# Kernel tuning notes

Measured on AMD Instinct MI355X. Metric: run time of the kernel, lower is better.

## Reference

```python
import jax, jax.numpy as jnp
import numpy as np

SEQ_LS = [512, 512, 512, 512]
HEADS = 8
DIM_HEAD = 64
DIM = 512
INNER = HEADS * DIM_HEAD  # 512
N = sum(SEQ_LS)           # 2048
B = 4
EPS = 1e-5

# static modality id per token position: [N]
MOD_IDS = jnp.asarray(np.repeat(np.arange(len(SEQ_LS)), SEQ_LS))


def setup_inputs() -> dict:
    key = jax.random.key(0)
    ks = jax.random.split(key, 6)
    x = jax.random.normal(ks[0], (B, N, DIM), dtype=jnp.float32)
    m_labels = jnp.ones((B, len(SEQ_LS)), dtype=jnp.int64 if jax.config.jax_enable_x64 else jnp.int32)
    gamma = jnp.ones((DIM,), dtype=jnp.float32)
    beta = jnp.zeros((DIM,), dtype=jnp.float32)
    w_qkv = jax.random.normal(ks[1], (DIM, 3 * INNER), dtype=jnp.float32) * (DIM ** -0.5)
    w_out = jax.random.normal(ks[2], (INNER, DIM), dtype=jnp.float32) * (INNER ** -0.5)
    b_out = jnp.zeros((DIM,), dtype=jnp.float32)
    return {"x": x, "m_labels": m_labels, "gamma": gamma, "beta": beta,
            "w_qkv": w_qkv, "w_out": w_out, "b_out": b_out}


def _additive_mask(m_labels):
    # present[b, n] = modality of token n is present in sample b
    present = (m_labels[:, MOD_IDS] != 0)                       # [B, N] bool
    pair_ok = present[:, :, None] & present[:, None, :]         # [B, N, N]
    neg_inf = jnp.float32(-jnp.inf)
    return jnp.where(pair_ok, jnp.float32(0.0), neg_inf)        # [B, N, N]


def reference(x, m_labels, gamma, beta, w_qkv, w_out, b_out):
    # LayerNorm(dim)
    mu = jnp.mean(x, axis=-1, keepdims=True)
    var = jnp.mean(jnp.square(x - mu), axis=-1, keepdims=True)
    xn = (x - mu) * jax.lax.rsqrt(var + EPS) * gamma + beta

    # QKV projection (no bias), split heads
    qkv = jnp.einsum('bnd,de->bne', xn, w_qkv)                  # [B, N, 3*INNER]
    q, k, v = jnp.split(qkv, 3, axis=-1)
    def heads(t):
        return t.reshape(B, N, HEADS, DIM_HEAD).transpose(0, 2, 1, 3)  # [B, H, N, Dh]
    q, k, v = heads(q), heads(k), heads(v)

    scale = DIM_HEAD ** -0.5
    dots = jnp.einsum('bhnd,bhmd->bhnm', q, k) * scale          # [B, H, N, N]
    dots = dots + _additive_mask(m_labels)[:, None, :, :]
    attn = jax.nn.softmax(dots, axis=-1)
    out = jnp.einsum('bhnm,bhmd->bhnd', attn, v)                # [B, H, N, Dh]
    out = out.transpose(0, 2, 1, 3).reshape(B, N, INNER)        # [B, N, INNER]
    return jnp.einsum('bni,io->bno', out, w_out) + b_out        # [B, N, DIM]
```

## Files before the change

kernel.cpp:

```cpp
#include <hip/hip_runtime.h>

#define DIMD 512
#define NTOK 2048
#define HEADS 8
#define DH 64

typedef __attribute__((ext_vector_type(4))) float f32x4;
typedef __attribute__((ext_vector_type(8))) __bf16 bf16x8;
typedef __attribute__((ext_vector_type(4))) short s16x4;

#define MFMA16(a, b, c) __builtin_amdgcn_mfma_f32_16x16x32_bf16((a), (b), (c), 0, 0, 0)
#define MFMAK16(a, b, c) __builtin_amdgcn_mfma_f32_16x16x16bf16_1k((a), (b), (c), 0, 0, 0)

__device__ __forceinline__ unsigned short f2bf(float f) {
  unsigned int u = __float_as_uint(f);
  u += 0x7fffu + ((u >> 16) & 1u);
  return (unsigned short)(u >> 16);
}

__device__ __forceinline__ unsigned packhi(float b, float a) {
  return (__float_as_uint(b) >> 16) | (__float_as_uint(a) & 0xffff0000u);
}

__device__ __forceinline__ void gl2lds16(const void* g, void* l) {
  auto gp = reinterpret_cast<__attribute__((address_space(1))) unsigned int*>(
      reinterpret_cast<unsigned long long>(g));
  auto lp = reinterpret_cast<__attribute__((address_space(3))) unsigned int*>(
      reinterpret_cast<unsigned long long>(l));
  __builtin_amdgcn_global_load_lds(gp, lp, 16, 0, 0);
}

__global__ __launch_bounds__(256) void ln_kernel(const float* __restrict__ x,
                                                 const float* __restrict__ gamma,
                                                 const float* __restrict__ beta,
                                                 unsigned short* __restrict__ xn) {
  const int row = blockIdx.x * 4 + (threadIdx.x >> 6);
  const int lane = threadIdx.x & 63;
  const float4* xr = (const float4*)(x + (size_t)row * DIMD);
  float4 a = xr[lane];
  float4 b = xr[lane + 64];
  float s = a.x + a.y + a.z + a.w + b.x + b.y + b.z + b.w;
  for (int off = 1; off < 64; off <<= 1) s += __shfl_xor(s, off, 64);
  float mu = s * (1.0f / DIMD);
  float d0 = a.x - mu, d1 = a.y - mu, d2 = a.z - mu, d3 = a.w - mu;
  float e0 = b.x - mu, e1 = b.y - mu, e2 = b.z - mu, e3 = b.w - mu;
  float v = d0 * d0 + d1 * d1 + d2 * d2 + d3 * d3 + e0 * e0 + e1 * e1 + e2 * e2 + e3 * e3;
  for (int off = 1; off < 64; off <<= 1) v += __shfl_xor(v, off, 64);
  float rs = rsqrtf(v * (1.0f / DIMD) + 1e-5f);
  const float4* g4 = (const float4*)gamma;
  const float4* be4 = (const float4*)beta;
  float4 ga = g4[lane], gb = g4[lane + 64];
  float4 ba = be4[lane], bb = be4[lane + 64];
  unsigned int p0 = (unsigned)f2bf(d0 * rs * ga.x + ba.x) | ((unsigned)f2bf(d1 * rs * ga.y + ba.y) << 16);
  unsigned int p1 = (unsigned)f2bf(d2 * rs * ga.z + ba.z) | ((unsigned)f2bf(d3 * rs * ga.w + ba.w) << 16);
  unsigned int p2 = (unsigned)f2bf(e0 * rs * gb.x + bb.x) | ((unsigned)f2bf(e1 * rs * gb.y + bb.y) << 16);
  unsigned int p3 = (unsigned)f2bf(e2 * rs * gb.z + bb.z) | ((unsigned)f2bf(e3 * rs * gb.w + bb.w) << 16);
  uint2 w0; w0.x = p0; w0.y = p1;
  uint2 w1; w1.x = p2; w1.y = p3;
  *(uint2*)&xn[(size_t)row * DIMD + lane * 4] = w0;
  *(uint2*)&xn[(size_t)row * DIMD + 256 + lane * 4] = w1;
}

__global__ __launch_bounds__(256) void wt_kernel(const float* __restrict__ w,
                                                 unsigned short* __restrict__ wt,
                                                 int R, int C) {
  __shared__ float t[32][33];
  int tx = threadIdx.x & 31, ty = threadIdx.x >> 5;
  int c0 = blockIdx.x * 32, r0 = blockIdx.y * 32;
  for (int i = 0; i < 4; i++)
    t[ty + 8 * i][tx] = w[(size_t)(r0 + ty + 8 * i) * C + c0 + tx];
  __syncthreads();
  for (int i = 0; i < 4; i++)
    wt[(size_t)(c0 + ty + 8 * i) * R + r0 + tx] = f2bf(t[tx][ty + 8 * i]);
}

__global__ __launch_bounds__(256, 2) void qkv_gemm(const unsigned short* __restrict__ A,
                                                   const unsigned short* __restrict__ Bt,
                                                   unsigned short* __restrict__ qb,
                                                   unsigned short* __restrict__ kb,
                                                   unsigned short* __restrict__ vtb) {
  __shared__ unsigned short As[2][128 * 64];
  __shared__ unsigned short Bs[2][128 * 64];
  const int tid = threadIdx.x;
  const int wave = tid >> 6, lane = tid & 63;
  const int row16 = lane & 15, quad = lane >> 4;
  const int rho = row16 & 7;
  const int m0 = blockIdx.x * 128;
  const int n0 = blockIdx.y * 128;
  const int rw = (wave & 1) * 64, cw = (wave >> 1) * 64;

  const char* Ab = (const char*)A;
  const char* Bb = (const char*)Bt;
#pragma unroll
  for (int i = 0; i < 4; i++) {
    int idx = i * 256 + tid;
    int r = idx >> 3;
    int c = (idx & 7) ^ (r & 7);
    gl2lds16(Ab + ((size_t)(m0 + r) * DIMD) * 2 + c * 16, (char*)As[0] + idx * 16);
    gl2lds16(Bb + ((size_t)(n0 + r) * DIMD) * 2 + c * 16, (char*)Bs[0] + idx * 16);
  }
  __syncthreads();

  f32x4 acc[4][4] = {};
  for (int kt = 0; kt < 8; kt++) {
    const int buf = kt & 1;
    if (kt < 7) {
      const int k0 = (kt + 1) * 64;
#pragma unroll
      for (int i = 0; i < 4; i++) {
        int idx = i * 256 + tid;
        int r = idx >> 3;
        int c = (idx & 7) ^ (r & 7);
        gl2lds16(Ab + ((size_t)(m0 + r) * DIMD + k0) * 2 + c * 16, (char*)As[buf ^ 1] + idx * 16);
        gl2lds16(Bb + ((size_t)(n0 + r) * DIMD + k0) * 2 + c * 16, (char*)Bs[buf ^ 1] + idx * 16);
      }
    }
#pragma unroll
    for (int ks = 0; ks < 2; ks++) {
      bf16x8 av[4], bv[4];
#pragma unroll
      for (int i = 0; i < 4; i++) {
        int Ra = rw + i * 16 + row16;
        int Rb = cw + i * 16 + row16;
        av[i] = *(const bf16x8*)&As[buf][Ra * 64 + (((ks * 4 + quad) ^ rho) * 8)];
        bv[i] = *(const bf16x8*)&Bs[buf][Rb * 64 + (((ks * 4 + quad) ^ rho) * 8)];
      }
#pragma unroll
      for (int i = 0; i < 4; i++)
#pragma unroll
        for (int j = 0; j < 4; j++) acc[i][j] = MFMA16(av[i], bv[j], acc[i][j]);
    }
    __syncthreads();
  }

  unsigned short* Ct = (unsigned short*)As;
#pragma unroll
  for (int i = 0; i < 4; i++)
#pragma unroll
    for (int j = 0; j < 4; j++)
#pragma unroll
      for (int r = 0; r < 4; r++)
        Ct[(rw + i * 16 + quad * 4 + r) * 136 + cw + j * 16 + row16] = f2bf(acc[i][j][r]);
  __syncthreads();

  const int sect = n0 >> 9;
  const int h0 = (n0 & 511) >> 6;
  const int b = m0 >> 11;
  const int nbase = m0 & 2047;
  if (sect < 2) {
    unsigned short* dst = (sect == 0) ? qb : kb;
#pragma unroll
    for (int i = 0; i < 8; i++) {
      int cid = i * 256 + tid;
      int row = cid >> 4, col0 = (cid & 15) * 8;
      int h = h0 + (col0 >> 6), d0 = col0 & 63;
      uint4 val = *(const uint4*)&Ct[row * 136 + col0];
      *(uint4*)&dst[(((size_t)(b * HEADS + h) * NTOK) + nbase + row) * DH + d0] = val;
    }
  } else {
#pragma unroll
    for (int u = 0; u < 4; u++) {
      int uid = u * 256 + tid;
      int col = uid >> 3, rc = (uid & 7) * 16;
      int h = h0 + (col >> 6), d = col & 63;
      unsigned short tmp[16];
#pragma unroll
      for (int j = 0; j < 16; j++) tmp[j] = Ct[(rc + j) * 136 + col];
      size_t base = ((size_t)(b * HEADS + h) * DH + d) * NTOK + nbase + rc;
      *(uint4*)&vtb[base] = *(uint4*)&tmp[0];
      *(uint4*)&vtb[base + 8] = *(uint4*)&tmp[8];
    }
  }
}

__global__ __launch_bounds__(256, 2) void attn_kernel(const unsigned short* __restrict__ qb,
                                                      const unsigned short* __restrict__ kb,
                                                      const unsigned short* __restrict__ vtb,
                                                      const int* __restrict__ mlab,
                                                      unsigned short* __restrict__ ao) {
  __shared__ unsigned short Qs[128 * 64];
  __shared__ unsigned short Ks[2][64 * 64];
  __shared__ unsigned short Vs[2][64 * 64];
  const int tid = threadIdx.x;
  const int wave = tid >> 6, lane = tid & 63;
  const int row16 = lane & 15, quad = lane >> 4;
  const int rho = row16 & 7;
  const int bh = blockIdx.y;
  const int b = bh >> 3, h = bh & 7;
  const int q0 = blockIdx.x * 128;

  const char* qg = (const char*)(qb + ((size_t)bh * NTOK + q0) * DH);
  const char* kgb = (const char*)(kb + (size_t)bh * NTOK * DH);
  const char* vgb = (const char*)(vtb + (size_t)bh * DH * NTOK);
  const int sr = tid >> 3;
  const int sc = (tid & 7) ^ (sr & 7);

#pragma unroll
  for (int i = 0; i < 4; i++)
    gl2lds16(qg + (sr + 32 * i) * 128 + sc * 16, (char*)Qs + tid * 16 + i * 4096);
  gl2lds16(kgb + sr * 128 + sc * 16, (char*)Ks[0] + tid * 16);
  gl2lds16(kgb + (sr + 32) * 128 + sc * 16, (char*)Ks[0] + tid * 16 + 4096);
  gl2lds16(vgb + (size_t)sr * 4096 + sc * 16, (char*)Vs[0] + tid * 16);
  gl2lds16(vgb + (size_t)(sr + 32) * 4096 + sc * 16, (char*)Vs[0] + tid * 16 + 4096);
  __syncthreads();

  bf16x8 aq[2][2];
#pragma unroll
  for (int qs = 0; qs < 2; qs++) {
    const int qrow = wave * 32 + qs * 16 + row16;
#pragma unroll
    for (int ki = 0; ki < 2; ki++)
      aq[qs][ki] = *(const bf16x8*)&Qs[qrow * 64 + (((ki * 4 + quad) ^ rho) * 8)];
  }

  f32x4 accT[4][2] = {};
  float lsum[2] = {0.f, 0.f};
  const float cs = 0.125f * 1.44269504088896f;
  const float c0 = mlab[b * 4 + 0] ? -16.f : -100000.f;
  const float c1 = mlab[b * 4 + 1] ? -16.f : -100000.f;
  const float c2 = mlab[b * 4 + 2] ? -16.f : -100000.f;
  const float c3 = mlab[b * 4 + 3] ? -16.f : -100000.f;

  for (int t = 0; t < 32; t++) {
    const int buf = t & 1;
    if (t < 31) {
      const char* kg = kgb + (size_t)(t + 1) * 8192;
      char* lk = (char*)Ks[buf ^ 1];
      gl2lds16(kg + sr * 128 + sc * 16, lk + tid * 16);
      gl2lds16(kg + (sr + 32) * 128 + sc * 16, lk + tid * 16 + 4096);
      const char* vg = vgb + (size_t)(t + 1) * 128;
      char* lv = (char*)Vs[buf ^ 1];
      gl2lds16(vg + (size_t)sr * 4096 + sc * 16, lv + tid * 16);
      gl2lds16(vg + (size_t)(sr + 32) * 4096 + sc * 16, lv + tid * 16 + 4096);
    }
    f32x4 S[2][4];
#pragma unroll
    for (int f = 0; f < 4; f++) {
      const unsigned short* Kr = &Ks[buf][(f * 16 + row16) * 64];
      bf16x8 ak0 = *(const bf16x8*)&Kr[(quad ^ rho) * 8];
      bf16x8 ak1 = *(const bf16x8*)&Kr[((quad + 4) ^ rho) * 8];
#pragma unroll
      for (int qs = 0; qs < 2; qs++) {
        f32x4 z = {};
        z = MFMA16(ak0, aq[qs][0], z);
        z = MFMA16(ak1, aq[qs][1], z);
        S[qs][f] = z;
      }
    }
    const int mi = t >> 3;
    const float c = (mi == 0) ? c0 : (mi == 1) ? c1 : (mi == 2) ? c2 : c3;
    s16x4 pf[2][4];
#pragma unroll
    for (int qs = 0; qs < 2; qs++)
#pragma unroll
      for (int f = 0; f < 4; f++) {
        float p0 = exp2f(fmaf(S[qs][f][0], cs, c));
        float p1 = exp2f(fmaf(S[qs][f][1], cs, c));
        float p2 = exp2f(fmaf(S[qs][f][2], cs, c));
        float p3 = exp2f(fmaf(S[qs][f][3], cs, c));
        lsum[qs] += (p0 + p1) + (p2 + p3);
        uint2 pk;
        pk.x = packhi(p0, p1);
        pk.y = packhi(p2, p3);
        pf[qs][f] = *(s16x4*)&pk;
      }
#pragma unroll
    for (int g = 0; g < 4; g++) {
      const unsigned short* Vr = &Vs[buf][(g * 16 + row16) * 64];
#pragma unroll
      for (int u = 0; u < 4; u++) {
        s16x4 va = *(const s16x4*)&Vr[(((2 * u + (quad >> 1)) ^ rho) * 8) + (quad & 1) * 4];
#pragma unroll
        for (int qs = 0; qs < 2; qs++) accT[g][qs] = MFMAK16(va, pf[qs][u], accT[g][qs]);
      }
    }
    __syncthreads();
  }

#pragma unroll
  for (int qs = 0; qs < 2; qs++) {
    float s = lsum[qs];
    s += __shfl_xor(s, 16, 64);
    s += __shfl_xor(s, 32, 64);
    lsum[qs] = 1.0f / s;
  }
#pragma unroll
  for (int qs = 0; qs < 2; qs++) {
    const int q = q0 + wave * 32 + qs * 16 + row16;
    unsigned short* aor = ao + ((size_t)b * NTOK + q) * DIMD + h * DH;
#pragma unroll
    for (int g = 0; g < 4; g++)
#pragma unroll
      for (int r = 0; r < 4; r++)
        aor[g * 16 + quad * 4 + r] = f2bf(accT[g][qs][r] * lsum[qs]);
  }
}

__global__ __launch_bounds__(256, 2) void out_gemm(const unsigned short* __restrict__ A,
                                                   const unsigned short* __restrict__ Bt,
                                                   const float* __restrict__ bias,
                                                   float* __restrict__ out) {
  __shared__ unsigned short As[2][128 * 64];
  __shared__ unsigned short Bs[2][128 * 64];
  const int tid = threadIdx.x;
  const int wave = tid >> 6, lane = tid & 63;
  const int row16 = lane & 15, quad = lane >> 4;
  const int rho = row16 & 7;
  const int m0 = blockIdx.x * 128;
  const int n0 = blockIdx.y * 128;
  const int rw = (wave & 1) * 64, cw = (wave >> 1) * 64;

  const char* Ab = (const char*)A;
  const char* Bb = (const char*)Bt;
#pragma unroll
  for (int i = 0; i < 4; i++) {
    int idx = i * 256 + tid;
    int r = idx >> 3;
    int c = (idx & 7) ^ (r & 7);
    gl2lds16(Ab + ((size_t)(m0 + r) * DIMD) * 2 + c * 16, (char*)As[0] + idx * 16);
    gl2lds16(Bb + ((size_t)(n0 + r) * DIMD) * 2 + c * 16, (char*)Bs[0] + idx * 16);
  }
  __syncthreads();

  f32x4 acc[4][4] = {};
  for (int kt = 0; kt < 8; kt++) {
    const int buf = kt & 1;
    if (kt < 7) {
      const int k0 = (kt + 1) * 64;
#pragma unroll
      for (int i = 0; i < 4; i++) {
        int idx = i * 256 + tid;
        int r = idx >> 3;
        int c = (idx & 7) ^ (r & 7);
        gl2lds16(Ab + ((size_t)(m0 + r) * DIMD + k0) * 2 + c * 16, (char*)As[buf ^ 1] + idx * 16);
        gl2lds16(Bb + ((size_t)(n0 + r) * DIMD + k0) * 2 + c * 16, (char*)Bs[buf ^ 1] + idx * 16);
      }
    }
#pragma unroll
    for (int ks = 0; ks < 2; ks++) {
      bf16x8 av[4], bv[4];
#pragma unroll
      for (int i = 0; i < 4; i++) {
        int Ra = rw + i * 16 + row16;
        int Rb = cw + i * 16 + row16;
        av[i] = *(const bf16x8*)&As[buf][Ra * 64 + (((ks * 4 + quad) ^ rho) * 8)];
        bv[i] = *(const bf16x8*)&Bs[buf][Rb * 64 + (((ks * 4 + quad) ^ rho) * 8)];
      }
#pragma unroll
      for (int i = 0; i < 4; i++)
#pragma unroll
        for (int j = 0; j < 4; j++) acc[i][j] = MFMA16(av[i], bv[j], acc[i][j]);
    }
    __syncthreads();
  }

#pragma unroll
  for (int j = 0; j < 4; j++) {
    const int col = n0 + cw + j * 16 + row16;
    const float bv = bias[col];
#pragma unroll
    for (int i = 0; i < 4; i++)
#pragma unroll
      for (int r = 0; r < 4; r++) {
        const int row = m0 + rw + i * 16 + quad * 4 + r;
        out[(size_t)row * DIMD + col] = acc[i][j][r] + bv;
      }
  }
}

extern "C" void kernel_launch(void* const* d_in, const int* in_sizes, int n_in,
                              void* d_out, int out_size, void* d_ws, size_t ws_size,
                              hipStream_t stream) {
  const float* x = (const float*)d_in[0];
  const int* mlab = (const int*)d_in[1];
  const float* gamma = (const float*)d_in[2];
  const float* beta = (const float*)d_in[3];
  const float* w_qkv = (const float*)d_in[4];
  const float* w_out = (const float*)d_in[5];
  const float* b_out = (const float*)d_in[6];
  float* out = (float*)d_out;

  char* ws = (char*)d_ws;
  unsigned short* xn = (unsigned short*)(ws);
  unsigned short* wqkvT = (unsigned short*)(ws + 8388608);
  unsigned short* woutT = (unsigned short*)(ws + 9961472);
  unsigned short* qbuf = (unsigned short*)(ws + 10485760);
  unsigned short* kbuf = (unsigned short*)(ws + 18874368);
  unsigned short* vtbuf = (unsigned short*)(ws + 27262976);
  unsigned short* aobuf = (unsigned short*)(ws + 35651584);

  ln_kernel<<<2048, 256, 0, stream>>>(x, gamma, beta, xn);
  wt_kernel<<<dim3(48, 16), 256, 0, stream>>>(w_qkv, wqkvT, 512, 1536);
  wt_kernel<<<dim3(16, 16), 256, 0, stream>>>(w_out, woutT, 512, 512);
  qkv_gemm<<<dim3(64, 12), 256, 0, stream>>>(xn, wqkvT, qbuf, kbuf, vtbuf);
  attn_kernel<<<dim3(16, 32), 256, 0, stream>>>(qbuf, kbuf, vtbuf, mlab, aobuf);
  out_gemm<<<dim3(64, 4), 256, 0, stream>>>(aobuf, woutT, b_out, out);
}
```

Before: 178.4 us.

## Split attention over key halves, merge prep kernels, and shrink out-GEMM tiles

Three launches (layernorm and two weight transposes) are merged into one prep kernel. Attention is split into two halves along the key axis, which doubles the grid and relies on the fixed -16 softmax offset so no max rescale is needed. The Q staging buffer is dropped so more blocks fit per CU, and a new combine kernel sums the partials and normalises. The output GEMM uses 128x64 tiles to launch more blocks. This costs an extra kernel, extra partial-output traffic, and truncating bf16 rounding of the unnormalised partials.

New measurement: 173.0 us. 1.03x faster.

```diff
diff --git a/kernel.cpp b/kernel.cpp
--- a/kernel.cpp
+++ b/kernel.cpp
@@ -21,6 +21,8 @@
 __device__ __forceinline__ unsigned packhi(float b, float a) {
   return (__float_as_uint(b) >> 16) | (__float_as_uint(a) & 0xffff0000u);
 }
+__device__ __forceinline__ float lo16(unsigned u) { return __uint_as_float(u << 16); }
+__device__ __forceinline__ float hi16(unsigned u) { return __uint_as_float(u & 0xffff0000u); }
 
 __device__ __forceinline__ void gl2lds16(const void* g, void* l) {
   auto gp = reinterpret_cast<__attribute__((address_space(1))) unsigned int*>(
@@ -30,48 +32,57 @@
   __builtin_amdgcn_global_load_lds(gp, lp, 16, 0, 0);
 }
 
-__global__ __launch_bounds__(256) void ln_kernel(const float* __restrict__ x,
-                                                 const float* __restrict__ gamma,
-                                                 const float* __restrict__ beta,
-                                                 unsigned short* __restrict__ xn) {
-  const int row = blockIdx.x * 4 + (threadIdx.x >> 6);
-  const int lane = threadIdx.x & 63;
-  const float4* xr = (const float4*)(x + (size_t)row * DIMD);
-  float4 a = xr[lane];
-  float4 b = xr[lane + 64];
-  float s = a.x + a.y + a.z + a.w + b.x + b.y + b.z + b.w;
-  for (int off = 1; off < 64; off <<= 1) s += __shfl_xor(s, off, 64);
-  float mu = s * (1.0f / DIMD);
-  float d0 = a.x - mu, d1 = a.y - mu, d2 = a.z - mu, d3 = a.w - mu;
-  float e0 = b.x - mu, e1 = b.y - mu, e2 = b.z - mu, e3 = b.w - mu;
-  float v = d0 * d0 + d1 * d1 + d2 * d2 + d3 * d3 + e0 * e0 + e1 * e1 + e2 * e2 + e3 * e3;
-  for (int off = 1; off < 64; off <<= 1) v += __shfl_xor(v, off, 64);
-  float rs = rsqrtf(v * (1.0f / DIMD) + 1e-5f);
-  const float4* g4 = (const float4*)gamma;
-  const float4* be4 = (const float4*)beta;
-  float4 ga = g4[lane], gb = g4[lane + 64];
-  float4 ba = be4[lane], bb = be4[lane + 64];
-  unsigned int p0 = (unsigned)f2bf(d0 * rs * ga.x + ba.x) | ((unsigned)f2bf(d1 * rs * ga.y + ba.y) << 16);
-  unsigned int p1 = (unsigned)f2bf(d2 * rs * ga.z + ba.z) | ((unsigned)f2bf(d3 * rs * ga.w + ba.w) << 16);
-  unsigned int p2 = (unsigned)f2bf(e0 * rs * gb.x + bb.x) | ((unsigned)f2bf(e1 * rs * gb.y + bb.y) << 16);
-  unsigned int p3 = (unsigned)f2bf(e2 * rs * gb.z + bb.z) | ((unsigned)f2bf(e3 * rs * gb.w + bb.w) << 16);
-  uint2 w0; w0.x = p0; w0.y = p1;
-  uint2 w1; w1.x = p2; w1.y = p3;
-  *(uint2*)&xn[(size_t)row * DIMD + lane * 4] = w0;
-  *(uint2*)&xn[(size_t)row * DIMD + 256 + lane * 4] = w1;
-}
-
-__global__ __launch_bounds__(256) void wt_kernel(const float* __restrict__ w,
-                                                 unsigned short* __restrict__ wt,
-                                                 int R, int C) {
+__global__ __launch_bounds__(256) void prep_kernel(const float* __restrict__ x,
+                                                   const float* __restrict__ gamma,
+                                                   const float* __restrict__ beta,
+                                                   const float* __restrict__ w_qkv,
+                                                   const float* __restrict__ w_out,
+                                                   unsigned short* __restrict__ xn,
+                                                   unsigned short* __restrict__ wqkvT,
+                                                   unsigned short* __restrict__ woutT) {
   __shared__ float t[32][33];
-  int tx = threadIdx.x & 31, ty = threadIdx.x >> 5;
-  int c0 = blockIdx.x * 32, r0 = blockIdx.y * 32;
-  for (int i = 0; i < 4; i++)
-    t[ty + 8 * i][tx] = w[(size_t)(r0 + ty + 8 * i) * C + c0 + tx];
-  __syncthreads();
-  for (int i = 0; i < 4; i++)
-    wt[(size_t)(c0 + ty + 8 * i) * R + r0 + tx] = f2bf(t[tx][ty + 8 * i]);
+  const int bid = blockIdx.x;
+  if (bid < 2048) {
+    const int row = bid * 4 + (threadIdx.x >> 6);
+    const int lane = threadIdx.x & 63;
+    const float4* xr = (const float4*)(x + (size_t)row * DIMD);
+    float4 a = xr[lane];
+    float4 b = xr[lane + 64];
+    float s = a.x + a.y + a.z + a.w + b.x + b.y + b.z + b.w;
+    for (int off = 1; off < 64; off <<= 1) s += __shfl_xor(s, off, 64);
+    float mu = s * (1.0f / DIMD);
+    float d0 = a.x - mu, d1 = a.y - mu, d2 = a.z - mu, d3 = a.w - mu;
+    float e0 = b.x - mu, e1 = b.y - mu, e2 = b.z - mu, e3 = b.w - mu;
+    float v = d0 * d0 + d1 * d1 + d2 * d2 + d3 * d3 + e0 * e0 + e1 * e1 + e2 * e2 + e3 * e3;
+    for (int off = 1; off < 64; off <<= 1) v += __shfl_xor(v, off, 64);
+    float rs = rsqrtf(v * (1.0f / DIMD) + 1e-5f);
+    const float4* g4 = (const float4*)gamma;
+    const float4* be4 = (const float4*)beta;
+    float4 ga = g4[lane], gb = g4[lane + 64];
+    float4 ba = be4[lane], bb = be4[lane + 64];
+    unsigned p0 = (unsigned)f2bf(d0 * rs * ga.x + ba.x) | ((unsigned)f2bf(d1 * rs * ga.y + ba.y) << 16);
+    unsigned p1 = (unsigned)f2bf(d2 * rs * ga.z + ba.z) | ((unsigned)f2bf(d3 * rs * ga.w + ba.w) << 16);
+    unsigned p2 = (unsigned)f2bf(e0 * rs * gb.x + bb.x) | ((unsigned)f2bf(e1 * rs * gb.y + bb.y) << 16);
+    unsigned p3 = (unsigned)f2bf(e2 * rs * gb.z + bb.z) | ((unsigned)f2bf(e3 * rs * gb.w + bb.w) << 16);
+    uint2 w0; w0.x = p0; w0.y = p1;
+    uint2 w1; w1.x = p2; w1.y = p3;
+    *(uint2*)&xn[(size_t)row * DIMD + lane * 4] = w0;
+    *(uint2*)&xn[(size_t)row * DIMD + 256 + lane * 4] = w1;
+  } else {
+    const float* w;
+    unsigned short* wt;
+    int C, bx, by;
+    if (bid < 2816) { w = w_qkv; wt = wqkvT; C = 1536; bx = (bid - 2048) % 48; by = (bid - 2048) / 48; }
+    else            { w = w_out; wt = woutT; C = 512;  bx = (bid - 2816) % 16; by = (bid - 2816) / 16; }
+    const int R = 512;
+    int tx = threadIdx.x & 31, ty = threadIdx.x >> 5;
+    int c0 = bx * 32, r0 = by * 32;
+    for (int i = 0; i < 4; i++)
+      t[ty + 8 * i][tx] = w[(size_t)(r0 + ty + 8 * i) * C + c0 + tx];
+    __syncthreads();
+    for (int i = 0; i < 4; i++)
+      wt[(size_t)(c0 + ty + 8 * i) * R + r0 + tx] = f2bf(t[tx][ty + 8 * i]);
+  }
 }
 
 __global__ __launch_bounds__(256, 2) void qkv_gemm(const unsigned short* __restrict__ A,
@@ -173,12 +184,13 @@
   }
 }
 
-__global__ __launch_bounds__(256, 2) void attn_kernel(const unsigned short* __restrict__ qb,
+__global__ __launch_bounds__(256, 4) void attn_kernel(const unsigned short* __restrict__ qb,
                                                       const unsigned short* __restrict__ kb,
                                                       const unsigned short* __restrict__ vtb,
                                                       const int* __restrict__ mlab,
-                                                      unsigned short* __restrict__ ao) {
-  __shared__ unsigned short Qs[128 * 64];
+                                                      unsigned short* __restrict__ aoP0,
+                                                      unsigned short* __restrict__ aoP1,
+                                                      float* __restrict__ lsumP) {
   __shared__ unsigned short Ks[2][64 * 64];
   __shared__ unsigned short Vs[2][64 * 64];
   const int tid = threadIdx.x;
@@ -186,44 +198,46 @@
   const int row16 = lane & 15, quad = lane >> 4;
   const int rho = row16 & 7;
   const int bh = blockIdx.y;
-  const int b = bh >> 3, h = bh & 7;
+  const int b = bh >> 3;
   const int q0 = blockIdx.x * 128;
+  const int kh = blockIdx.z;
 
   const char* qg = (const char*)(qb + ((size_t)bh * NTOK + q0) * DH);
-  const char* kgb = (const char*)(kb + (size_t)bh * NTOK * DH);
-  const char* vgb = (const char*)(vtb + (size_t)bh * DH * NTOK);
+  const char* kgb = (const char*)(kb + ((size_t)bh * NTOK + kh * 1024) * DH);
+  const char* vgb = (const char*)(vtb + (size_t)bh * DH * NTOK + kh * 1024);
   const int sr = tid >> 3;
   const int sc = (tid & 7) ^ (sr & 7);
 
-#pragma unroll
-  for (int i = 0; i < 4; i++)
-    gl2lds16(qg + (sr + 32 * i) * 128 + sc * 16, (char*)Qs + tid * 16 + i * 4096);
+  gl2lds16(qg + sr * 128 + sc * 16, (char*)Ks[1] + tid * 16);
+  gl2lds16(qg + (sr + 32) * 128 + sc * 16, (char*)Ks[1] + tid * 16 + 4096);
+  gl2lds16(qg + (sr + 64) * 128 + sc * 16, (char*)Vs[1] + tid * 16);
+  gl2lds16(qg + (sr + 96) * 128 + sc * 16, (char*)Vs[1] + tid * 16 + 4096);
   gl2lds16(kgb + sr * 128 + sc * 16, (char*)Ks[0] + tid * 16);
   gl2lds16(kgb + (sr + 32) * 128 + sc * 16, (char*)Ks[0] + tid * 16 + 4096);
   gl2lds16(vgb + (size_t)sr * 4096 + sc * 16, (char*)Vs[0] + tid * 16);
   gl2lds16(vgb + (size_t)(sr + 32) * 4096 + sc * 16, (char*)Vs[0] + tid * 16 + 4096);
   __syncthreads();
 
+  const unsigned short* Qbase = (wave < 2) ? Ks[1] : Vs[1];
   bf16x8 aq[2][2];
 #pragma unroll
   for (int qs = 0; qs < 2; qs++) {
-    const int qrow = wave * 32 + qs * 16 + row16;
+    const int rowb = (wave & 1) * 32 + qs * 16 + row16;
 #pragma unroll
     for (int ki = 0; ki < 2; ki++)
-      aq[qs][ki] = *(const bf16x8*)&Qs[qrow * 64 + (((ki * 4 + quad) ^ rho) * 8)];
-  }
+      aq[qs][ki] = *(const bf16x8*)&Qbase[rowb * 64 + (((ki * 4 + quad) ^ rho) * 8)];
+  }
+  __syncthreads();
 
   f32x4 accT[4][2] = {};
   float lsum[2] = {0.f, 0.f};
   const float cs = 0.125f * 1.44269504088896f;
-  const float c0 = mlab[b * 4 + 0] ? -16.f : -100000.f;
-  const float c1 = mlab[b * 4 + 1] ? -16.f : -100000.f;
-  const float c2 = mlab[b * 4 + 2] ? -16.f : -100000.f;
-  const float c3 = mlab[b * 4 + 3] ? -16.f : -100000.f;
-
-  for (int t = 0; t < 32; t++) {
+  const float cA = mlab[b * 4 + kh * 2] ? -16.f : -100000.f;
+  const float cB = mlab[b * 4 + kh * 2 + 1] ? -16.f : -100000.f;
+
+  for (int t = 0; t < 16; t++) {
     const int buf = t & 1;
-    if (t < 31) {
+    if (t < 15) {
       const char* kg = kgb + (size_t)(t + 1) * 8192;
       char* lk = (char*)Ks[buf ^ 1];
       gl2lds16(kg + sr * 128 + sc * 16, lk + tid * 16);
@@ -247,8 +261,7 @@
         S[qs][f] = z;
       }
     }
-    const int mi = t >> 3;
-    const float c = (mi == 0) ? c0 : (mi == 1) ? c1 : (mi == 2) ? c2 : c3;
+    const float c = (t < 8) ? cA : cB;
     s16x4 pf[2][4];
 #pragma unroll
     for (int qs = 0; qs < 2; qs++)
@@ -282,18 +295,49 @@
     float s = lsum[qs];
     s += __shfl_xor(s, 16, 64);
     s += __shfl_xor(s, 32, 64);
-    lsum[qs] = 1.0f / s;
-  }
+    lsum[qs] = s;
+  }
+  float* lsP = lsumP + (size_t)kh * 65536 + (size_t)bh * 2048 + q0;
+  if (quad == 0) {
+    lsP[wave * 32 + row16] = lsum[0];
+    lsP[wave * 32 + 16 + row16] = lsum[1];
+  }
+  unsigned short* aoPk = (kh == 0) ? aoP0 : aoP1;
 #pragma unroll
   for (int qs = 0; qs < 2; qs++) {
-    const int q = q0 + wave * 32 + qs * 16 + row16;
-    unsigned short* aor = ao + ((size_t)b * NTOK + q) * DIMD + h * DH;
-#pragma unroll
-    for (int g = 0; g < 4; g++)
-#pragma unroll
-      for (int r = 0; r < 4; r++)
-        aor[g * 16 + quad * 4 + r] = f2bf(accT[g][qs][r] * lsum[qs]);
-  }
+    const int q = wave * 32 + qs * 16 + row16;
+    unsigned short* dst = aoPk + ((size_t)bh * NTOK + q0 + q) * DH;
+#pragma unroll
+    for (int g = 0; g < 4; g++) {
+      *(unsigned*)&dst[g * 16 + quad * 4] = packhi(accT[g][qs][0], accT[g][qs][1]);
+      *(unsigned*)&dst[g * 16 + quad * 4 + 2] = packhi(accT[g][qs][2], accT[g][qs][3]);
+    }
+  }
+}
+
+__global__ __launch_bounds__(256) void combine_kernel(const unsigned short* __restrict__ aoP0,
+                                                      const unsigned short* __restrict__ aoP1,
+                                                      const float* __restrict__ lsumP,
+                                                      unsigned short* __restrict__ ao) {
+  const int idx = blockIdx.x * 256 + threadIdx.x;
+  const int d0 = (idx & 7) * 8;
+  const int h = (idx >> 3) & 7;
+  const int n = (idx >> 6) & 2047;
+  const int b = idx >> 17;
+  const size_t bhn = ((size_t)(b * 8 + h)) * 2048 + n;
+  const uint4 u1 = *(const uint4*)&aoP0[bhn * 64 + d0];
+  const uint4 u2 = *(const uint4*)&aoP1[bhn * 64 + d0];
+  const float inv = 1.0f / (lsumP[bhn] + lsumP[65536 + bhn]);
+  const unsigned* a1 = (const unsigned*)&u1;
+  const unsigned* a2 = (const unsigned*)&u2;
+  unsigned o[4];
+#pragma unroll
+  for (int k = 0; k < 4; k++) {
+    float e0 = (lo16(a1[k]) + lo16(a2[k])) * inv;
+    float e1 = (hi16(a1[k]) + hi16(a2[k])) * inv;
+    o[k] = (unsigned)f2bf(e0) | ((unsigned)f2bf(e1) << 16);
+  }
+  *(uint4*)&ao[(((size_t)b * 2048 + n) * 512) + h * 64 + d0] = *(uint4*)o;
 }
 
 __global__ __launch_bounds__(256, 2) void out_gemm(const unsigned short* __restrict__ A,
@@ -301,14 +345,14 @@
                                                    const float* __restrict__ bias,
                                                    float* __restrict__ out) {
   __shared__ unsigned short As[2][128 * 64];
-  __shared__ unsigned short Bs[2][128 * 64];
+  __shared__ unsigned short Bs[2][64 * 64];
   const int tid = threadIdx.x;
   const int wave = tid >> 6, lane = tid & 63;
   const int row16 = lane & 15, quad = lane >> 4;
   const int rho = row16 & 7;
   const int m0 = blockIdx.x * 128;
-  const int n0 = blockIdx.y * 128;
-  const int rw = (wave & 1) * 64, cw = (wave >> 1) * 64;
+  const int n0 = blockIdx.y * 64;
+  const int rw = (wave & 1) * 64, cw = (wave >> 1) * 32;
 
   const char* Ab = (const char*)A;
   const char* Bb = (const char*)Bt;
@@ -318,11 +362,17 @@
     int r = idx >> 3;
     int c = (idx & 7) ^ (r & 7);
     gl2lds16(Ab + ((size_t)(m0 + r) * DIMD) * 2 + c * 16, (char*)As[0] + idx * 16);
+  }
+#pragma unroll
+  for (int i = 0; i < 2; i++) {
+    int idx = i * 256 + tid;
+    int r = idx >> 3;
+    int c = (idx & 7) ^ (r & 7);
     gl2lds16(Bb + ((size_t)(n0 + r) * DIMD) * 2 + c * 16, (char*)Bs[0] + idx * 16);
   }
   __syncthreads();
 
-  f32x4 acc[4][4] = {};
+  f32x4 acc[4][2] = {};
   for (int kt = 0; kt < 8; kt++) {
     const int buf = kt & 1;
     if (kt < 7) {
@@ -333,29 +383,34 @@
         int r = idx >> 3;
         int c = (idx & 7) ^ (r & 7);
         gl2lds16(Ab + ((size_t)(m0 + r) * DIMD + k0) * 2 + c * 16, (char*)As[buf ^ 1] + idx * 16);
+      }
+#pragma unroll
+      for (int i = 0; i < 2; i++) {
+        int idx = i * 256 + tid;
+        int r = idx >> 3;
+        int c = (idx & 7) ^ (r & 7);
         gl2lds16(Bb + ((size_t)(n0 + r) * DIMD + k0) * 2 + c * 16, (char*)Bs[buf ^ 1] + idx * 16);
       }
     }
 #pragma unroll
     for (int ks = 0; ks < 2; ks++) {
-      bf16x8 av[4], bv[4];
-#pragma unroll
-      for (int i = 0; i < 4; i++) {
-        int Ra = rw + i * 16 + row16;
-        int Rb = cw + i * 16 + row16;
-        av[i] = *(const bf16x8*)&As[buf][Ra * 64 + (((ks * 4 + quad) ^ rho) * 8)];
-        bv[i] = *(const bf16x8*)&Bs[buf][Rb * 64 + (((ks * 4 + quad) ^ rho) * 8)];
-      }
+      bf16x8 av[4], bv[2];
 #pragma unroll
       for (int i = 0; i < 4; i++)
-#pragma unroll
-        for (int j = 0; j < 4; j++) acc[i][j] = MFMA16(av[i], bv[j], acc[i][j]);
+        av[i] = *(const bf16x8*)&As[buf][(rw + i * 16 + row16) * 64 + (((ks * 4 + quad) ^ rho) * 8)];
+#pragma unroll
+      for (int j = 0; j < 2; j++)
+        bv[j] = *(const bf16x8*)&Bs[buf][(cw + j * 16 + row16) * 64 + (((ks * 4 + quad) ^ rho) * 8)];
+#pragma unroll
+      for (int i = 0; i < 4; i++)
+#pragma unroll
+        for (int j = 0; j < 2; j++) acc[i][j] = MFMA16(av[i], bv[j], acc[i][j]);
     }
     __syncthreads();
   }
 
 #pragma unroll
-  for (int j = 0; j < 4; j++) {
+  for (int j = 0; j < 2; j++) {
     const int col = n0 + cw + j * 16 + row16;
     const float bv = bias[col];
 #pragma unroll
@@ -387,12 +442,14 @@
   unsigned short* qbuf = (unsigned short*)(ws + 10485760);
   unsigned short* kbuf = (unsigned short*)(ws + 18874368);
   unsigned short* vtbuf = (unsigned short*)(ws + 27262976);
-  unsigned short* aobuf = (unsigned short*)(ws + 35651584);
-
-  ln_kernel<<<2048, 256, 0, stream>>>(x, gamma, beta, xn);
-  wt_kernel<<<dim3(48, 16), 256, 0, stream>>>(w_qkv, wqkvT, 512, 1536);
-  wt_kernel<<<dim3(16, 16), 256, 0, stream>>>(w_out, woutT, 512, 512);
+  unsigned short* aoP1 = (unsigned short*)(ws + 35651584);
+  unsigned short* aoP0 = xn;
+  float* lsumP = (float*)wqkvT;
+  unsigned short* ao8 = qbuf;
+
+  prep_kernel<<<3072, 256, 0, stream>>>(x, gamma, beta, w_qkv, w_out, xn, wqkvT, woutT);
   qkv_gemm<<<dim3(64, 12), 256, 0, stream>>>(xn, wqkvT, qbuf, kbuf, vtbuf);
-  attn_kernel<<<dim3(16, 32), 256, 0, stream>>>(qbuf, kbuf, vtbuf, mlab, aobuf);
-  out_gemm<<<dim3(64, 4), 256, 0, stream>>>(aobuf, woutT, b_out, out);
-}
+  attn_kernel<<<dim3(16, 32, 2), 256, 0, stream>>>(qbuf, kbuf, vtbuf, mlab, aoP0, aoP1, lsumP);
+  combine_kernel<<<2048, 256, 0, stream>>>(aoP0, aoP1, lsumP, ao8);
+  out_gemm<<<dim3(64, 8), 256, 0, stream>>>(ao8, woutT, b_out, out);
+}
```

## Fuse prep kernels, compute softmax row sums via MFMA, shrink out_gemm tile

Applied to the files above, without the earlier changes.

Merges the LayerNorm and the two weight-transpose kernels into one launch, which removes two launch gaps. In attention, the per-lane exp sum and its cross-lane shuffles are replaced by an MFMA against a vector of ones, and the bf16 output stores become packed 32-bit writes that use perm-based truncation. out_gemm uses 128x64 tiles so it launches 512 blocks instead of 256, giving better CU occupancy. The trade-offs are extra MFMA work per tile, and the attention output now truncates to bf16 instead of rounding.

After: 170.2 us. 1.05x faster.

```diff
diff --git a/kernel.cpp b/kernel.cpp
--- a/kernel.cpp
+++ b/kernel.cpp
@@ -19,7 +19,11 @@
 }
 
 __device__ __forceinline__ unsigned packhi(float b, float a) {
+#if __has_builtin(__builtin_amdgcn_perm)
+  return __builtin_amdgcn_perm(__float_as_uint(a), __float_as_uint(b), 0x07060302u);
+#else
   return (__float_as_uint(b) >> 16) | (__float_as_uint(a) & 0xffff0000u);
+#endif
 }
 
 __device__ __forceinline__ void gl2lds16(const void* g, void* l) {
@@ -30,48 +34,57 @@
   __builtin_amdgcn_global_load_lds(gp, lp, 16, 0, 0);
 }
 
-__global__ __launch_bounds__(256) void ln_kernel(const float* __restrict__ x,
-                                                 const float* __restrict__ gamma,
-                                                 const float* __restrict__ beta,
-                                                 unsigned short* __restrict__ xn) {
-  const int row = blockIdx.x * 4 + (threadIdx.x >> 6);
-  const int lane = threadIdx.x & 63;
-  const float4* xr = (const float4*)(x + (size_t)row * DIMD);
-  float4 a = xr[lane];
-  float4 b = xr[lane + 64];
-  float s = a.x + a.y + a.z + a.w + b.x + b.y + b.z + b.w;
-  for (int off = 1; off < 64; off <<= 1) s += __shfl_xor(s, off, 64);
-  float mu = s * (1.0f / DIMD);
-  float d0 = a.x - mu, d1 = a.y - mu, d2 = a.z - mu, d3 = a.w - mu;
-  float e0 = b.x - mu, e1 = b.y - mu, e2 = b.z - mu, e3 = b.w - mu;
-  float v = d0 * d0 + d1 * d1 + d2 * d2 + d3 * d3 + e0 * e0 + e1 * e1 + e2 * e2 + e3 * e3;
-  for (int off = 1; off < 64; off <<= 1) v += __shfl_xor(v, off, 64);
-  float rs = rsqrtf(v * (1.0f / DIMD) + 1e-5f);
-  const float4* g4 = (const float4*)gamma;
-  const float4* be4 = (const float4*)beta;
-  float4 ga = g4[lane], gb = g4[lane + 64];
-  float4 ba = be4[lane], bb = be4[lane + 64];
-  unsigned int p0 = (unsigned)f2bf(d0 * rs * ga.x + ba.x) | ((unsigned)f2bf(d1 * rs * ga.y + ba.y) << 16);
-  unsigned int p1 = (unsigned)f2bf(d2 * rs * ga.z + ba.z) | ((unsigned)f2bf(d3 * rs * ga.w + ba.w) << 16);
-  unsigned int p2 = (unsigned)f2bf(e0 * rs * gb.x + bb.x) | ((unsigned)f2bf(e1 * rs * gb.y + bb.y) << 16);
-  unsigned int p3 = (unsigned)f2bf(e2 * rs * gb.z + bb.z) | ((unsigned)f2bf(e3 * rs * gb.w + bb.w) << 16);
-  uint2 w0; w0.x = p0; w0.y = p1;
-  uint2 w1; w1.x = p2; w1.y = p3;
-  *(uint2*)&xn[(size_t)row * DIMD + lane * 4] = w0;
-  *(uint2*)&xn[(size_t)row * DIMD + 256 + lane * 4] = w1;
-}
-
-__global__ __launch_bounds__(256) void wt_kernel(const float* __restrict__ w,
-                                                 unsigned short* __restrict__ wt,
-                                                 int R, int C) {
+__global__ __launch_bounds__(256) void prep_kernel(const float* __restrict__ x,
+                                                   const float* __restrict__ gamma,
+                                                   const float* __restrict__ beta,
+                                                   const float* __restrict__ w_qkv,
+                                                   const float* __restrict__ w_out,
+                                                   unsigned short* __restrict__ xn,
+                                                   unsigned short* __restrict__ wqkvT,
+                                                   unsigned short* __restrict__ woutT) {
   __shared__ float t[32][33];
-  int tx = threadIdx.x & 31, ty = threadIdx.x >> 5;
-  int c0 = blockIdx.x * 32, r0 = blockIdx.y * 32;
-  for (int i = 0; i < 4; i++)
-    t[ty + 8 * i][tx] = w[(size_t)(r0 + ty + 8 * i) * C + c0 + tx];
-  __syncthreads();
-  for (int i = 0; i < 4; i++)
-    wt[(size_t)(c0 + ty + 8 * i) * R + r0 + tx] = f2bf(t[tx][ty + 8 * i]);
+  const int bid = blockIdx.x;
+  if (bid < 2048) {
+    const int row = bid * 4 + (threadIdx.x >> 6);
+    const int lane = threadIdx.x & 63;
+    const float4* xr = (const float4*)(x + (size_t)row * DIMD);
+    float4 a = xr[lane];
+    float4 b = xr[lane + 64];
+    float s = a.x + a.y + a.z + a.w + b.x + b.y + b.z + b.w;
+    for (int off = 1; off < 64; off <<= 1) s += __shfl_xor(s, off, 64);
+    float mu = s * (1.0f / DIMD);
+    float d0 = a.x - mu, d1 = a.y - mu, d2 = a.z - mu, d3 = a.w - mu;
+    float e0 = b.x - mu, e1 = b.y - mu, e2 = b.z - mu, e3 = b.w - mu;
+    float v = d0 * d0 + d1 * d1 + d2 * d2 + d3 * d3 + e0 * e0 + e1 * e1 + e2 * e2 + e3 * e3;
+    for (int off = 1; off < 64; off <<= 1) v += __shfl_xor(v, off, 64);
+    float rs = rsqrtf(v * (1.0f / DIMD) + 1e-5f);
+    const float4* g4 = (const float4*)gamma;
+    const float4* be4 = (const float4*)beta;
+    float4 ga = g4[lane], gb = g4[lane + 64];
+    float4 ba = be4[lane], bb = be4[lane + 64];
+    unsigned p0 = (unsigned)f2bf(d0 * rs * ga.x + ba.x) | ((unsigned)f2bf(d1 * rs * ga.y + ba.y) << 16);
+    unsigned p1 = (unsigned)f2bf(d2 * rs * ga.z + ba.z) | ((unsigned)f2bf(d3 * rs * ga.w + ba.w) << 16);
+    unsigned p2 = (unsigned)f2bf(e0 * rs * gb.x + bb.x) | ((unsigned)f2bf(e1 * rs * gb.y + bb.y) << 16);
+    unsigned p3 = (unsigned)f2bf(e2 * rs * gb.z + bb.z) | ((unsigned)f2bf(e3 * rs * gb.w + bb.w) << 16);
+    uint2 w0; w0.x = p0; w0.y = p1;
+    uint2 w1; w1.x = p2; w1.y = p3;
+    *(uint2*)&xn[(size_t)row * DIMD + lane * 4] = w0;
+    *(uint2*)&xn[(size_t)row * DIMD + 256 + lane * 4] = w1;
+  } else {
+    const float* w;
+    unsigned short* wt;
+    int C, bx, by;
+    if (bid < 2816) { w = w_qkv; wt = wqkvT; C = 1536; bx = (bid - 2048) % 48; by = (bid - 2048) / 48; }
+    else            { w = w_out; wt = woutT; C = 512;  bx = (bid - 2816) % 16; by = (bid - 2816) / 16; }
+    const int R = 512;
+    int tx = threadIdx.x & 31, ty = threadIdx.x >> 5;
+    int c0 = bx * 32, r0 = by * 32;
+    for (int i = 0; i < 4; i++)
+      t[ty + 8 * i][tx] = w[(size_t)(r0 + ty + 8 * i) * C + c0 + tx];
+    __syncthreads();
+    for (int i = 0; i < 4; i++)
+      wt[(size_t)(c0 + ty + 8 * i) * R + r0 + tx] = f2bf(t[tx][ty + 8 * i]);
+  }
 }
 
 __global__ __launch_bounds__(256, 2) void qkv_gemm(const unsigned short* __restrict__ A,
@@ -213,8 +226,11 @@
       aq[qs][ki] = *(const bf16x8*)&Qs[qrow * 64 + (((ki * 4 + quad) ^ rho) * 8)];
   }
 
+  s16x4 onesf;
+  onesf[0] = onesf[1] = onesf[2] = onesf[3] = (short)0x3F80;
+
   f32x4 accT[4][2] = {};
-  float lsum[2] = {0.f, 0.f};
+  f32x4 accL[2] = {};
   const float cs = 0.125f * 1.44269504088896f;
   const float c0 = mlab[b * 4 + 0] ? -16.f : -100000.f;
   const float c1 = mlab[b * 4 + 1] ? -16.f : -100000.f;
@@ -258,7 +274,6 @@
         float p1 = exp2f(fmaf(S[qs][f][1], cs, c));
         float p2 = exp2f(fmaf(S[qs][f][2], cs, c));
         float p3 = exp2f(fmaf(S[qs][f][3], cs, c));
-        lsum[qs] += (p0 + p1) + (p2 + p3);
         uint2 pk;
         pk.x = packhi(p0, p1);
         pk.y = packhi(p2, p3);
@@ -274,25 +289,25 @@
         for (int qs = 0; qs < 2; qs++) accT[g][qs] = MFMAK16(va, pf[qs][u], accT[g][qs]);
       }
     }
+#pragma unroll
+    for (int u = 0; u < 4; u++)
+#pragma unroll
+      for (int qs = 0; qs < 2; qs++) accL[qs] = MFMAK16(onesf, pf[qs][u], accL[qs]);
     __syncthreads();
   }
 
-#pragma unroll
-  for (int qs = 0; qs < 2; qs++) {
-    float s = lsum[qs];
-    s += __shfl_xor(s, 16, 64);
-    s += __shfl_xor(s, 32, 64);
-    lsum[qs] = 1.0f / s;
-  }
+  float inv[2];
+  inv[0] = 1.0f / accL[0][0];
+  inv[1] = 1.0f / accL[1][0];
 #pragma unroll
   for (int qs = 0; qs < 2; qs++) {
     const int q = q0 + wave * 32 + qs * 16 + row16;
     unsigned short* aor = ao + ((size_t)b * NTOK + q) * DIMD + h * DH;
 #pragma unroll
-    for (int g = 0; g < 4; g++)
-#pragma unroll
-      for (int r = 0; r < 4; r++)
-        aor[g * 16 + quad * 4 + r] = f2bf(accT[g][qs][r] * lsum[qs]);
+    for (int g = 0; g < 4; g++) {
+      *(unsigned*)&aor[g * 16 + quad * 4] = packhi(accT[g][qs][0] * inv[qs], accT[g][qs][1] * inv[qs]);
+      *(unsigned*)&aor[g * 16 + quad * 4 + 2] = packhi(accT[g][qs][2] * inv[qs], accT[g][qs][3] * inv[qs]);
+    }
   }
 }
 
@@ -301,14 +316,14 @@
                                                    const float* __restrict__ bias,
                                                    float* __restrict__ out) {
   __shared__ unsigned short As[2][128 * 64];
-  __shared__ unsigned short Bs[2][128 * 64];
+  __shared__ unsigned short Bs[2][64 * 64];
   const int tid = threadIdx.x;
   const int wave = tid >> 6, lane = tid & 63;
   const int row16 = lane & 15, quad = lane >> 4;
   const int rho = row16 & 7;
   const int m0 = blockIdx.x * 128;
-  const int n0 = blockIdx.y * 128;
-  const int rw = (wave & 1) * 64, cw = (wave >> 1) * 64;
+  const int n0 = blockIdx.y * 64;
+  const int rw = (wave & 1) * 64, cw = (wave >> 1) * 32;
 
   const char* Ab = (const char*)A;
   const char* Bb = (const char*)Bt;
@@ -318,11 +333,17 @@
     int r = idx >> 3;
     int c = (idx & 7) ^ (r & 7);
     gl2lds16(Ab + ((size_t)(m0 + r) * DIMD) * 2 + c * 16, (char*)As[0] + idx * 16);
+  }
+#pragma unroll
+  for (int i = 0; i < 2; i++) {
+    int idx = i * 256 + tid;
+    int r = idx >> 3;
+    int c = (idx & 7) ^ (r & 7);
     gl2lds16(Bb + ((size_t)(n0 + r) * DIMD) * 2 + c * 16, (char*)Bs[0] + idx * 16);
   }
   __syncthreads();
 
-  f32x4 acc[4][4] = {};
+  f32x4 acc[4][2] = {};
   for (int kt = 0; kt < 8; kt++) {
     const int buf = kt & 1;
     if (kt < 7) {
@@ -333,29 +354,34 @@
         int r = idx >> 3;
         int c = (idx & 7) ^ (r & 7);
         gl2lds16(Ab + ((size_t)(m0 + r) * DIMD + k0) * 2 + c * 16, (char*)As[buf ^ 1] + idx * 16);
+      }
+#pragma unroll
+      for (int i = 0; i < 2; i++) {
+        int idx = i * 256 + tid;
+        int r = idx >> 3;
+        int c = (idx & 7) ^ (r & 7);
         gl2lds16(Bb + ((size_t)(n0 + r) * DIMD + k0) * 2 + c * 16, (char*)Bs[buf ^ 1] + idx * 16);
       }
     }
 #pragma unroll
     for (int ks = 0; ks < 2; ks++) {
-      bf16x8 av[4], bv[4];
-#pragma unroll
-      for (int i = 0; i < 4; i++) {
-        int Ra = rw + i * 16 + row16;
-        int Rb = cw + i * 16 + row16;
-        av[i] = *(const bf16x8*)&As[buf][Ra * 64 + (((ks * 4 + quad) ^ rho) * 8)];
-        bv[i] = *(const bf16x8*)&Bs[buf][Rb * 64 + (((ks * 4 + quad) ^ rho) * 8)];
-      }
+      bf16x8 av[4], bv[2];
 #pragma unroll
       for (int i = 0; i < 4; i++)
-#pragma unroll
-        for (int j = 0; j < 4; j++) acc[i][j] = MFMA16(av[i], bv[j], acc[i][j]);
+        av[i] = *(const bf16x8*)&As[buf][(rw + i * 16 + row16) * 64 + (((ks * 4 + quad) ^ rho) * 8)];
+#pragma unroll
+      for (int j = 0; j < 2; j++)
+        bv[j] = *(const bf16x8*)&Bs[buf][(cw + j * 16 + row16) * 64 + (((ks * 4 + quad) ^ rho) * 8)];
+#pragma unroll
+      for (int i = 0; i < 4; i++)
+#pragma unroll
+        for (int j = 0; j < 2; j++) acc[i][j] = MFMA16(av[i], bv[j], acc[i][j]);
     }
     __syncthreads();
   }
 
 #pragma unroll
-  for (int j = 0; j < 4; j++) {
+  for (int j = 0; j < 2; j++) {
     const int col = n0 + cw + j * 16 + row16;
     const float bv = bias[col];
 #pragma unroll
@@ -389,10 +415,8 @@
   unsigned short* vtbuf = (unsigned short*)(ws + 27262976);
   unsigned short* aobuf = (unsigned short*)(ws + 35651584);
 
-  ln_kernel<<<2048, 256, 0, stream>>>(x, gamma, beta, xn);
-  wt_kernel<<<dim3(48, 16), 256, 0, stream>>>(w_qkv, wqkvT, 512, 1536);
-  wt_kernel<<<dim3(16, 16), 256, 0, stream>>>(w_out, woutT, 512, 512);
+  prep_kernel<<<3072, 256, 0, stream>>>(x, gamma, beta, w_qkv, w_out, xn, wqkvT, woutT);
   qkv_gemm<<<dim3(64, 12), 256, 0, stream>>>(xn, wqkvT, qbuf, kbuf, vtbuf);
   attn_kernel<<<dim3(16, 32), 256, 0, stream>>>(qbuf, kbuf, vtbuf, mlab, aobuf);
-  out_gemm<<<dim3(64, 4), 256, 0, stream>>>(aobuf, woutT, b_out, out);
-}
+  out_gemm<<<dim3(64, 8), 256, 0, stream>>>(aobuf, woutT, b_out, out);
+}
```
